# Performance work log

Hardware: AMD Instinct MI355X
Metric: run time of the kernel (lower is better)

The kernel has to match this reference:

```python
import jax, jax.numpy as jnp
import numpy as np

QP = 127.0          # signed symmetric 8-bit: Qp = 2**(8-1)-1
MIN_RANGE = 1e-6


def _ste_round(q):
    # round_pass: straight-through estimator round
    return q + jax.lax.stop_gradient(jnp.round(q) - q)


def _quant_per_token(x):
    # symmetric per-token: amax over last dim, keepdim
    s = jnp.clip(jnp.max(jnp.abs(x), axis=-1, keepdims=True), MIN_RANGE, None) / QP
    return _ste_round(x / s), s


def _quant_per_tensor(w):
    s = jnp.clip(jnp.max(jnp.abs(w)), MIN_RANGE, None) / QP
    return _ste_round(w / s), s


def _qlinear(x2d, w, b):
    # fake-quant linear: quantize act per-token, weight per-tensor,
    # int-domain matmul, bias added before dequant rescale (faithful to source)
    qx, sx = _quant_per_token(x2d)      # [N,K], [N,1]
    qw, sw = _quant_per_tensor(w)       # [M,K], scalar
    out = jnp.matmul(qx, qw.T) + b[None, :]
    return out * (sx * sw)              # [N,M]


def setup_inputs() -> dict:
    key = jax.random.key(0)
    k1, k2, k3, k4, k5 = jax.random.split(key, 5)
    B, S, D, H = 64, 197, 768, 3072
    return {
        "x": jax.random.normal(k1, (B, S, D), dtype=jnp.float32),
        "w1": jax.random.normal(k2, (H, D), dtype=jnp.float32) * 0.02,
        "b1": jax.random.normal(k3, (H,), dtype=jnp.float32) * 0.02,
        "w2": jax.random.normal(k4, (D, H), dtype=jnp.float32) * 0.02,
        "b2": jax.random.normal(k5, (D,), dtype=jnp.float32) * 0.02,
    }


def reference(x, w1, b1, w2, b2):
    B, S, D = x.shape
    x2d = x.reshape(-1, D)                         # view(-1, x.size(-1))
    h = _qlinear(x2d, w1, b1)                      # fc1
    h = jax.nn.gelu(h, approximate=False)          # ViT Mlp activation (exact GELU)
    o = _qlinear(h, w2, b2)                        # fc2
    return o.reshape(B, S, -1)
```

## Files before the change

### kernel.cpp

```cpp
#include <hip/hip_runtime.h>
#include <stdint.h>

#define QPF  127.0f
#define MINR 1e-6f

typedef int v4i __attribute__((ext_vector_type(4)));
typedef _Float16 h8 __attribute__((ext_vector_type(8)));
typedef signed char c8 __attribute__((ext_vector_type(8)));

__device__ __forceinline__ float wave_max64(float v) {
  v = fmaxf(v, __shfl_xor(v, 32, 64));
  v = fmaxf(v, __shfl_xor(v, 16, 64));
  v = fmaxf(v, __shfl_xor(v, 8, 64));
  v = fmaxf(v, __shfl_xor(v, 4, 64));
  v = fmaxf(v, __shfl_xor(v, 2, 64));
  v = fmaxf(v, __shfl_xor(v, 1, 64));
  return v;
}

__device__ __forceinline__ float gelu_exact(float x) {
  float z = fabsf(x) * 0.70710678118654752440f;
  float t = __builtin_amdgcn_rcpf(fmaf(0.3275911f, z, 1.0f));
  float p = fmaf(fmaf(fmaf(fmaf(1.061405429f, t, -1.453152027f), t,
                           1.421413741f), t, -0.284496736f), t, 0.254829592f) * t;
  float e = __expf(-z * z);
  float erfz = fmaf(-p, e, 1.0f);
  float cdf = fmaf(0.5f, copysignf(erfz, x), 0.5f);
  return x * cdf;
}

__device__ __forceinline__ void gl2lds16(const void* g, void* l) {
  __builtin_amdgcn_global_load_lds(
      (const __attribute__((address_space(1))) int*)g,
      (__attribute__((address_space(3))) int*)l,
      16, 0, 0);
}

__global__ __launch_bounds__(256) void amax_kernel(const float* __restrict__ w,
                                                   int n4, unsigned* out) {
  const float4* w4 = (const float4*)w;
  float m = 0.f;
  for (int i = blockIdx.x * blockDim.x + threadIdx.x; i < n4;
       i += gridDim.x * blockDim.x) {
    float4 v = w4[i];
    m = fmaxf(m, fmaxf(fmaxf(fabsf(v.x), fabsf(v.y)),
                       fmaxf(fabsf(v.z), fabsf(v.w))));
  }
  m = wave_max64(m);
  __shared__ float red[4];
  const int lane = threadIdx.x & 63, wv = threadIdx.x >> 6;
  if (lane == 0) red[wv] = m;
  __syncthreads();
  if (threadIdx.x == 0) {
    float mm = fmaxf(fmaxf(red[0], red[1]), fmaxf(red[2], red[3]));
    atomicMax(out, __float_as_uint(mm));
  }
}

__global__ __launch_bounds__(256) void wquant_kernel(const float* __restrict__ w,
                                                     int n4,
                                                     const unsigned* __restrict__ amaxbits,
                                                     signed char* __restrict__ q) {
  const float s = fmaxf(__uint_as_float(*amaxbits), MINR) / QPF;
  const float rs = 1.0f / s;
  const float4* w4 = (const float4*)w;
  char4* q4 = (char4*)q;
  for (int i = blockIdx.x * blockDim.x + threadIdx.x; i < n4;
       i += gridDim.x * blockDim.x) {
    float4 v = w4[i];
    char4 c;
    c.x = (signed char)(int)rintf(v.x * rs);
    c.y = (signed char)(int)rintf(v.y * rs);
    c.z = (signed char)(int)rintf(v.z * rs);
    c.w = (signed char)(int)rintf(v.w * rs);
    q4[i] = c;
  }
}

__global__ __launch_bounds__(256) void xquant_kernel(const float* __restrict__ x,
                                                     signed char* __restrict__ qx,
                                                     float* __restrict__ sx, int K) {
  const int token = blockIdx.x;
  const float4* xr = (const float4*)(x + (size_t)token * K);
  const int k4 = K >> 2;
  float m = 0.f;
  for (int i = threadIdx.x; i < k4; i += 256) {
    float4 v = xr[i];
    m = fmaxf(m, fmaxf(fmaxf(fabsf(v.x), fabsf(v.y)),
                       fmaxf(fabsf(v.z), fabsf(v.w))));
  }
  m = wave_max64(m);
  __shared__ float red[4];
  const int lane = threadIdx.x & 63, wv = threadIdx.x >> 6;
  if (lane == 0) red[wv] = m;
  __syncthreads();
  const float M = fmaxf(fmaxf(red[0], red[1]), fmaxf(red[2], red[3]));
  const float s = fmaxf(M, MINR) / QPF;
  const float rs = 1.0f / s;
  if (threadIdx.x == 0) sx[token] = s;
  char4* qr = (char4*)(qx + (size_t)token * K);
  for (int i = threadIdx.x; i < k4; i += 256) {
    float4 v = xr[i];
    char4 c;
    c.x = (signed char)(int)rintf(v.x * rs);
    c.y = (signed char)(int)rintf(v.y * rs);
    c.z = (signed char)(int)rintf(v.z * rs);
    c.w = (signed char)(int)rintf(v.w * rs);
    qr[i] = c;
  }
}

__global__ __launch_bounds__(256) void hquant_kernel(const _Float16* __restrict__ h,
                                                     const unsigned* __restrict__ amaxbits,
                                                     signed char* __restrict__ qh,
                                                     float* __restrict__ sh, int K) {
  const int token = blockIdx.x;
  const float s = fmaxf(__uint_as_float(amaxbits[token]), MINR) / QPF;
  const float rs = 1.0f / s;
  if (threadIdx.x == 0) sh[token] = s;
  const h8* hr = (const h8*)(h + (size_t)token * K);
  c8* qr = (c8*)(qh + (size_t)token * K);
  for (int i = threadIdx.x; i < (K >> 3); i += 256) {
    h8 v = hr[i];
    c8 c;
#pragma unroll
    for (int j = 0; j < 8; j++)
      c[j] = (signed char)(int)rintf((float)v[j] * rs);
    qr[i] = c;
  }
}

template <bool GELU_EPI>
__global__ __launch_bounds__(256, 2) void gemm_i8(
    const signed char* __restrict__ A,
    const signed char* __restrict__ B,
    const float* __restrict__ bias,
    const float* __restrict__ sA,
    const unsigned* __restrict__ sBbits,
    void* __restrict__ outv,
    unsigned* __restrict__ amax_out,
    int N, int K, int Mout) {
  __shared__ __align__(16) signed char As[2 * 128 * 64];
  __shared__ __align__(16) signed char Bs[2 * 128 * 64];

  const int t = threadIdx.x;
  const int lane = t & 63;
  const int wv = t >> 6;
  const int wm = wv >> 1;
  const int wn = wv & 1;
  const int rowBlk = blockIdx.y * 128;
  const int colBlk = blockIdx.x * 128;

  int ar0 = rowBlk + wv * 16 + (lane >> 2);
  int ar1 = ar0 + 64;
  if (ar0 > N - 1) ar0 = N - 1;
  if (ar1 > N - 1) ar1 = N - 1;
  const int br0 = colBlk + wv * 16 + (lane >> 2);
  const int br1 = br0 + 64;
  const int kb = (((lane & 3) ^ ((lane >> 3) & 3)) * 16);

  const signed char* gA0 = A + (size_t)ar0 * K + kb;
  const signed char* gA1 = A + (size_t)ar1 * K + kb;
  const signed char* gB0 = B + (size_t)br0 * K + kb;
  const signed char* gB1 = B + (size_t)br1 * K + kb;

  const v4i vzero = {0, 0, 0, 0};
  v4i acc[4][4];
#pragma unroll
  for (int i = 0; i < 4; i++)
#pragma unroll
    for (int j = 0; j < 4; j++) acc[i][j] = vzero;

  const int swz = ((lane >> 4) ^ ((lane >> 1) & 3)) * 16;
  const int aoff = (wm * 64 + (lane & 15)) * 64 + swz;
  const int boff = (wn * 64 + (lane & 15)) * 64 + swz;

  const int T = K >> 6;

  {
    signed char* a = As + wv * 1024;
    signed char* b = Bs + wv * 1024;
    gl2lds16(gA0, a);
    gl2lds16(gA1, a + 4096);
    gl2lds16(gB0, b);
    gl2lds16(gB1, b + 4096);
    gA0 += 64; gA1 += 64; gB0 += 64; gB1 += 64;
  }

  int buf = 0;
  for (int kt = 0; kt < T; ++kt) {
    __syncthreads();
    if (kt + 1 < T) {
      const int o = (buf ^ 1) * 8192;
      signed char* a = As + o + wv * 1024;
      signed char* b = Bs + o + wv * 1024;
      gl2lds16(gA0, a);
      gl2lds16(gA1, a + 4096);
      gl2lds16(gB0, b);
      gl2lds16(gB1, b + 4096);
      gA0 += 64; gA1 += 64; gB0 += 64; gB1 += 64;
    }
    const int o = buf * 8192;
    v4i a[4], b[4];
#pragma unroll
    for (int mi = 0; mi < 4; mi++) a[mi] = *(const v4i*)(As + o + aoff + mi * 1024);
#pragma unroll
    for (int ni = 0; ni < 4; ni++) b[ni] = *(const v4i*)(Bs + o + boff + ni * 1024);
#pragma unroll
    for (int mi = 0; mi < 4; mi++)
#pragma unroll
      for (int ni = 0; ni < 4; ni++)
        acc[mi][ni] = __builtin_amdgcn_mfma_i32_16x16x64_i8(a[mi], b[ni],
                                                            acc[mi][ni], 0, 0, 0);
    buf ^= 1;
  }

  const float sB = fmaxf(__uint_as_float(*sBbits), MINR) / QPF;
  const int colb = colBlk + wn * 64 + (lane & 15);
  const int rowb = rowBlk + wm * 64 + (lane >> 4) * 4;

  float bv[4];
#pragma unroll
  for (int ni = 0; ni < 4; ni++) bv[ni] = bias[colb + ni * 16];

#pragma unroll
  for (int mi = 0; mi < 4; mi++) {
    const int row0 = rowb + mi * 16;
    float sAv[4];
#pragma unroll
    for (int r = 0; r < 4; r++) sAv[r] = (row0 + r < N) ? sA[row0 + r] : 0.f;
    float rmax[4] = {0.f, 0.f, 0.f, 0.f};
#pragma unroll
    for (int ni = 0; ni < 4; ni++) {
#pragma unroll
      for (int r = 0; r < 4; r++) {
        float v = ((float)acc[mi][ni][r] + bv[ni]) * (sAv[r] * sB);
        if (GELU_EPI) v = gelu_exact(v);
        rmax[r] = fmaxf(rmax[r], fabsf(v));
        if (row0 + r < N) {
          const size_t idx = (size_t)(row0 + r) * Mout + colb + ni * 16;
          if (GELU_EPI)
            ((_Float16*)outv)[idx] = (_Float16)v;
          else
            ((float*)outv)[idx] = v;
        }
      }
    }
    if (GELU_EPI) {
#pragma unroll
      for (int r = 0; r < 4; r++) {
        float m = rmax[r];
        m = fmaxf(m, __shfl_xor(m, 1, 64));
        m = fmaxf(m, __shfl_xor(m, 2, 64));
        m = fmaxf(m, __shfl_xor(m, 4, 64));
        m = fmaxf(m, __shfl_xor(m, 8, 64));
        if ((lane & 15) == 0 && row0 + r < N)
          atomicMax(amax_out + row0 + r, __float_as_uint(m));
      }
    }
  }
}

extern "C" void kernel_launch(void* const* d_in, const int* in_sizes, int n_in,
                              void* d_out, int out_size, void* d_ws, size_t ws_size,
                              hipStream_t stream) {
  const float* x  = (const float*)d_in[0];
  const float* w1 = (const float*)d_in[1];
  const float* b1 = (const float*)d_in[2];
  const float* w2 = (const float*)d_in[3];
  const float* b2 = (const float*)d_in[4];

  const int H = in_sizes[2];
  const int D = in_sizes[4];
  const int N = in_sizes[0] / D;
  float* out = (float*)d_out;

  char* ws = (char*)d_ws;
  auto alloc = [&](size_t bytes) {
    char* p = ws;
    ws += (bytes + 255) & ~(size_t)255;
    return p;
  };
  signed char* qx  = (signed char*)alloc((size_t)N * D);
  signed char* qw1 = (signed char*)alloc((size_t)H * D);
  signed char* qw2 = (signed char*)alloc((size_t)H * D);
  signed char* qh  = (signed char*)alloc((size_t)N * H);
  float*    sx     = (float*)alloc((size_t)N * 4);
  float*    sh     = (float*)alloc((size_t)N * 4);
  unsigned* amaxh  = (unsigned*)alloc((size_t)N * 4);
  unsigned* wamax  = (unsigned*)alloc(256);
  _Float16* h      = (_Float16*)alloc((size_t)N * H * 2);
  (void)ws_size;

  hipMemsetAsync(amaxh, 0, (size_t)N * 4, stream);
  hipMemsetAsync(wamax, 0, 8, stream);

  const int n4w = (H * D) >> 2;
  amax_kernel<<<512, 256, 0, stream>>>(w1, n4w, wamax + 0);
  amax_kernel<<<512, 256, 0, stream>>>(w2, n4w, wamax + 1);
  wquant_kernel<<<1024, 256, 0, stream>>>(w1, n4w, wamax + 0, qw1);
  wquant_kernel<<<1024, 256, 0, stream>>>(w2, n4w, wamax + 1, qw2);
  xquant_kernel<<<N, 256, 0, stream>>>(x, qx, sx, D);

  dim3 g1(H / 128, (N + 127) / 128);
  gemm_i8<true><<<g1, 256, 0, stream>>>(qx, qw1, b1, sx, wamax + 0, (void*)h,
                                        amaxh, N, D, H);
  hquant_kernel<<<N, 256, 0, stream>>>(h, amaxh, qh, sh, H);

  dim3 g2(D / 128, (N + 127) / 128);
  gemm_i8<false><<<g2, 256, 0, stream>>>(qh, qw2, b2, sh, wamax + 1, (void*)out,
                                         nullptr, N, H, D);
}
```

Measured before the change: 272.3 us.

## Triple-buffer GEMM LDS pipeline and merge weight quant and memset launches

The int8 GEMM moves from a double-buffered LDS scheme to a three-stage ring buffer. Each iteration uses explicit vmcnt waits and a raw barrier, so two tiles are in flight while the current one is computed. Separately, the two weight amax and quant kernels are merged into single launches using blockIdx.y, the two memsets are merged into one, and the per-token quant kernels drop to one wave per block with no shared-memory reduction. The aim is to hide global-to-LDS latency and cut launch overhead. The cost is 48KB of LDS per block, which may reduce occupancy, and waitcnt encodings that are written by hand.

```diff
diff --git a/kernel.cpp b/kernel.cpp
--- a/kernel.cpp
+++ b/kernel.cpp
@@ -36,9 +36,10 @@
       16, 0, 0);
 }
 
-__global__ __launch_bounds__(256) void amax_kernel(const float* __restrict__ w,
-                                                   int n4, unsigned* out) {
-  const float4* w4 = (const float4*)w;
+__global__ __launch_bounds__(256) void amax2_kernel(const float* __restrict__ w1,
+                                                    const float* __restrict__ w2,
+                                                    int n4, unsigned* out) {
+  const float4* w4 = (const float4*)(blockIdx.y ? w2 : w1);
   float m = 0.f;
   for (int i = blockIdx.x * blockDim.x + threadIdx.x; i < n4;
        i += gridDim.x * blockDim.x) {
@@ -53,18 +54,20 @@
   __syncthreads();
   if (threadIdx.x == 0) {
     float mm = fmaxf(fmaxf(red[0], red[1]), fmaxf(red[2], red[3]));
-    atomicMax(out, __float_as_uint(mm));
-  }
-}
-
-__global__ __launch_bounds__(256) void wquant_kernel(const float* __restrict__ w,
-                                                     int n4,
-                                                     const unsigned* __restrict__ amaxbits,
-                                                     signed char* __restrict__ q) {
-  const float s = fmaxf(__uint_as_float(*amaxbits), MINR) / QPF;
+    atomicMax(out + blockIdx.y, __float_as_uint(mm));
+  }
+}
+
+__global__ __launch_bounds__(256) void wquant2_kernel(const float* __restrict__ w1,
+                                                      const float* __restrict__ w2,
+                                                      int n4,
+                                                      const unsigned* __restrict__ amaxbits,
+                                                      signed char* __restrict__ q1,
+                                                      signed char* __restrict__ q2) {
+  const float4* w4 = (const float4*)(blockIdx.y ? w2 : w1);
+  char4* q4 = (char4*)(blockIdx.y ? q2 : q1);
+  const float s = fmaxf(__uint_as_float(amaxbits[blockIdx.y]), MINR) / QPF;
   const float rs = 1.0f / s;
-  const float4* w4 = (const float4*)w;
-  char4* q4 = (char4*)q;
   for (int i = blockIdx.x * blockDim.x + threadIdx.x; i < n4;
        i += gridDim.x * blockDim.x) {
     float4 v = w4[i];
@@ -77,29 +80,25 @@
   }
 }
 
-__global__ __launch_bounds__(256) void xquant_kernel(const float* __restrict__ x,
-                                                     signed char* __restrict__ qx,
-                                                     float* __restrict__ sx, int K) {
+__global__ __launch_bounds__(64) void xquant_kernel(const float* __restrict__ x,
+                                                    signed char* __restrict__ qx,
+                                                    float* __restrict__ sx, int K) {
   const int token = blockIdx.x;
   const float4* xr = (const float4*)(x + (size_t)token * K);
   const int k4 = K >> 2;
+  const int lane = threadIdx.x;
   float m = 0.f;
-  for (int i = threadIdx.x; i < k4; i += 256) {
+  for (int i = lane; i < k4; i += 64) {
     float4 v = xr[i];
     m = fmaxf(m, fmaxf(fmaxf(fabsf(v.x), fabsf(v.y)),
                        fmaxf(fabsf(v.z), fabsf(v.w))));
   }
   m = wave_max64(m);
-  __shared__ float red[4];
-  const int lane = threadIdx.x & 63, wv = threadIdx.x >> 6;
-  if (lane == 0) red[wv] = m;
-  __syncthreads();
-  const float M = fmaxf(fmaxf(red[0], red[1]), fmaxf(red[2], red[3]));
-  const float s = fmaxf(M, MINR) / QPF;
+  const float s = fmaxf(m, MINR) / QPF;
   const float rs = 1.0f / s;
-  if (threadIdx.x == 0) sx[token] = s;
+  if (lane == 0) sx[token] = s;
   char4* qr = (char4*)(qx + (size_t)token * K);
-  for (int i = threadIdx.x; i < k4; i += 256) {
+  for (int i = lane; i < k4; i += 64) {
     float4 v = xr[i];
     char4 c;
     c.x = (signed char)(int)rintf(v.x * rs);
@@ -110,17 +109,17 @@
   }
 }
 
-__global__ __launch_bounds__(256) void hquant_kernel(const _Float16* __restrict__ h,
-                                                     const unsigned* __restrict__ amaxbits,
-                                                     signed char* __restrict__ qh,
-                                                     float* __restrict__ sh, int K) {
+__global__ __launch_bounds__(64) void hquant_kernel(const _Float16* __restrict__ h,
+                                                    const unsigned* __restrict__ amaxbits,
+                                                    signed char* __restrict__ qh,
+                                                    float* __restrict__ sh, int K) {
   const int token = blockIdx.x;
   const float s = fmaxf(__uint_as_float(amaxbits[token]), MINR) / QPF;
   const float rs = 1.0f / s;
   if (threadIdx.x == 0) sh[token] = s;
   const h8* hr = (const h8*)(h + (size_t)token * K);
   c8* qr = (c8*)(qh + (size_t)token * K);
-  for (int i = threadIdx.x; i < (K >> 3); i += 256) {
+  for (int i = threadIdx.x; i < (K >> 3); i += 64) {
     h8 v = hr[i];
     c8 c;
 #pragma unroll
@@ -140,8 +139,7 @@
     void* __restrict__ outv,
     unsigned* __restrict__ amax_out,
     int N, int K, int Mout) {
-  __shared__ __align__(16) signed char As[2 * 128 * 64];
-  __shared__ __align__(16) signed char Bs[2 * 128 * 64];
+  __shared__ __align__(16) signed char lds[3 * 16384];
 
   const int t = threadIdx.x;
   const int lane = t & 63;
@@ -173,46 +171,53 @@
 
   const int swz = ((lane >> 4) ^ ((lane >> 1) & 3)) * 16;
   const int aoff = (wm * 64 + (lane & 15)) * 64 + swz;
-  const int boff = (wn * 64 + (lane & 15)) * 64 + swz;
+  const int boff = (wn * 64 + (lane & 15)) * 64 + swz + 8192;
 
   const int T = K >> 6;
 
-  {
-    signed char* a = As + wv * 1024;
-    signed char* b = Bs + wv * 1024;
+  auto issue = [&](int bufo) {
+    signed char* a = lds + bufo + wv * 1024;
     gl2lds16(gA0, a);
     gl2lds16(gA1, a + 4096);
-    gl2lds16(gB0, b);
-    gl2lds16(gB1, b + 4096);
+    gl2lds16(gB0, a + 8192);
+    gl2lds16(gB1, a + 12288);
     gA0 += 64; gA1 += 64; gB0 += 64; gB1 += 64;
-  }
-
-  int buf = 0;
+  };
+
+  issue(0);
+  if (T > 1) issue(16384);
+
+  int cur = 0;
   for (int kt = 0; kt < T; ++kt) {
-    __syncthreads();
-    if (kt + 1 < T) {
-      const int o = (buf ^ 1) * 8192;
-      signed char* a = As + o + wv * 1024;
-      signed char* b = Bs + o + wv * 1024;
-      gl2lds16(gA0, a);
-      gl2lds16(gA1, a + 4096);
-      gl2lds16(gB0, b);
-      gl2lds16(gB1, b + 4096);
-      gA0 += 64; gA1 += 64; gB0 += 64; gB1 += 64;
+    asm volatile("" ::: "memory");
+    if (kt < T - 1)
+      __builtin_amdgcn_s_waitcnt(0x0074);
+    else
+      __builtin_amdgcn_s_waitcnt(0x0070);
+    __builtin_amdgcn_s_barrier();
+    asm volatile("" ::: "memory");
+
+    if (kt + 2 < T) {
+      int pf = cur + 32768;
+      if (pf >= 49152) pf -= 49152;
+      issue(pf);
     }
-    const int o = buf * 8192;
+
     v4i a[4], b[4];
 #pragma unroll
-    for (int mi = 0; mi < 4; mi++) a[mi] = *(const v4i*)(As + o + aoff + mi * 1024);
-#pragma unroll
-    for (int ni = 0; ni < 4; ni++) b[ni] = *(const v4i*)(Bs + o + boff + ni * 1024);
+    for (int mi = 0; mi < 4; mi++)
+      a[mi] = *(const v4i*)(lds + cur + aoff + mi * 1024);
+#pragma unroll
+    for (int ni = 0; ni < 4; ni++)
+      b[ni] = *(const v4i*)(lds + cur + boff + ni * 1024);
 #pragma unroll
     for (int mi = 0; mi < 4; mi++)
 #pragma unroll
       for (int ni = 0; ni < 4; ni++)
         acc[mi][ni] = __builtin_amdgcn_mfma_i32_16x16x64_i8(a[mi], b[ni],
                                                             acc[mi][ni], 0, 0, 0);
-    buf ^= 1;
+    cur += 16384;
+    if (cur >= 49152) cur = 0;
   }
 
   const float sB = fmaxf(__uint_as_float(*sBbits), MINR) / QPF;
@@ -292,20 +297,17 @@
   _Float16* h      = (_Float16*)alloc((size_t)N * H * 2);
   (void)ws_size;
 
-  hipMemsetAsync(amaxh, 0, (size_t)N * 4, stream);
-  hipMemsetAsync(wamax, 0, 8, stream);
+  hipMemsetAsync(amaxh, 0, (((size_t)N * 4 + 255) & ~(size_t)255) + 256, stream);
 
   const int n4w = (H * D) >> 2;
-  amax_kernel<<<512, 256, 0, stream>>>(w1, n4w, wamax + 0);
-  amax_kernel<<<512, 256, 0, stream>>>(w2, n4w, wamax + 1);
-  wquant_kernel<<<1024, 256, 0, stream>>>(w1, n4w, wamax + 0, qw1);
-  wquant_kernel<<<1024, 256, 0, stream>>>(w2, n4w, wamax + 1, qw2);
-  xquant_kernel<<<N, 256, 0, stream>>>(x, qx, sx, D);
+  amax2_kernel<<<dim3(512, 2), 256, 0, stream>>>(w1, w2, n4w, wamax);
+  wquant2_kernel<<<dim3(1024, 2), 256, 0, stream>>>(w1, w2, n4w, wamax, qw1, qw2);
+  xquant_kernel<<<N, 64, 0, stream>>>(x, qx, sx, D);
 
   dim3 g1(H / 128, (N + 127) / 128);
   gemm_i8<true><<<g1, 256, 0, stream>>>(qx, qw1, b1, sx, wamax + 0, (void*)h,
                                         amaxh, N, D, H);
-  hquant_kernel<<<N, 256, 0, stream>>>(h, amaxh, qh, sh, H);
+  hquant_kernel<<<N, 64, 0, stream>>>(h, amaxh, qh, sh, H);
 
   dim3 g2(D / 128, (N + 127) / 128);
   gemm_i8<false><<<g2, 256, 0, stream>>>(qh, qw2, b2, sh, wamax + 1, (void*)out,
```

Result: faster. 266.3 us (-2.2%).
